# Optimization experiments

Measured on AMD Instinct MI355X. Metric: run time of the kernel, lower is better.

Reference implementation:

```python
import jax, jax.numpy as jnp
import numpy as np

SEQ = 110          # input_size1 = sample_width*2
HALF = SEQ // 2    # 55
N_EMBD = 102       # n_chrom + 2
HEAD = 192

def _cross_half_mask():
    # attention allowed only between the two halves (same-half blocks masked)
    idx = jnp.arange(SEQ)
    same_half = (idx[:, None] < HALF) == (idx[None, :] < HALF)
    return same_half  # True where attention is DISALLOWED

def setup_inputs() -> dict:
    key = jax.random.key(0)
    k1, k2, k3, k4 = jax.random.split(key, 4)
    B = 8192
    x = jax.random.normal(k1, (B, SEQ, N_EMBD), dtype=jnp.float32)
    Wq = jax.random.normal(k2, (N_EMBD, HEAD), dtype=jnp.float32) * (N_EMBD ** -0.5)
    Wk = jax.random.normal(k3, (N_EMBD, HEAD), dtype=jnp.float32) * (N_EMBD ** -0.5)
    Wv = jax.random.normal(k4, (N_EMBD, HEAD), dtype=jnp.float32) * (N_EMBD ** -0.5)
    return {"x": x, "Wq": Wq, "Wk": Wk, "Wv": Wv}

def reference(x, Wq, Wk, Wv):
    # q,k,v: [B, S, H]
    q = x @ Wq
    k = x @ Wk
    v = x @ Wv
    scale = HEAD ** -0.5
    scores = jnp.einsum('bsh,bth->bst', q, k) * scale  # [B, S, S]
    mask = _cross_half_mask()                           # [S, S] True = masked
    scores = jnp.where(mask, -jnp.inf, scores)
    attn = jax.nn.softmax(scores, axis=-1)
    # dropout is identity at inference (p=0.15 at train)
    out = jnp.einsum('bst,bth->bsh', attn, v)           # [B, S, H]
    return out
```

## Files before the change

kernel.cpp:

```cpp
#include <hip/hip_runtime.h>
#include <hip/hip_bf16.h>

#define SEQ   110
#define HALFS 55
#define EMB   102
#define HEAD  192

typedef short bf16x8 __attribute__((ext_vector_type(8)));
typedef float f32x4  __attribute__((ext_vector_type(4)));

#define XS    104
#define XTILE (64 * XS)
#define PS    72
#define MTS   128
#define MTROWS 112
#define MT_SHORTS (MTROWS * MTS)
#define WES   128

__device__ __forceinline__ short f2bf(float f) {
    unsigned u = __float_as_uint(f);
    unsigned r = u + 0x7fffu + ((u >> 16) & 1u);
    return (short)(r >> 16);
}
__device__ __forceinline__ unsigned pk2(float a, float b) {
    return ((unsigned)(unsigned short)f2bf(b) << 16) | (unsigned short)f2bf(a);
}

__global__ void prep(const float* __restrict__ Wq, const float* __restrict__ Wk,
                     const float* __restrict__ Wv, short* __restrict__ ws) {
    int flat = blockIdx.x * 256 + threadIdx.x;
    if (flat < MT_SHORTS) {
        int i = flat >> 7, j = flat & 127;
        float v = 0.0f;
        if (i < EMB && j < EMB) {
            const float4* q4 = (const float4*)(Wq + j * HEAD);
            const float4* k4 = (const float4*)(Wk + i * HEAD);
            float s = 0.0f;
            #pragma unroll 4
            for (int h4 = 0; h4 < HEAD / 4; ++h4) {
                float4 a = q4[h4], b = k4[h4];
                s += a.x * b.x + a.y * b.y + a.z * b.z + a.w * b.w;
            }
            v = s * 0.07216878364870322f;
        }
        ws[flat] = f2bf(v);
    } else if (flat < MT_SHORTS + HEAD * WES) {
        int idx = flat - MT_SHORTS;
        int h = idx >> 7, e = idx & 127;
        float v = (e < EMB) ? Wv[e * HEAD + h] : 0.0f;
        ws[flat] = f2bf(v);
    }
}

__global__ __launch_bounds__(256, 2)
void attn_head(const float* __restrict__ x, const short* __restrict__ ws,
               float* __restrict__ out, int B) {
    const int tid  = threadIdx.x;
    const int w    = tid >> 6;
    const int lane = tid & 63;
    const int g    = lane >> 4;
    const int r    = lane & 15;

    __shared__ __attribute__((aligned(16))) short u[3 * XTILE];
    __shared__ __attribute__((aligned(16))) short P_lds[64 * PS];
    short* slotA = u;
    short* slotB = u + XTILE;
    short* slotC = u + 2 * XTILE;

    const short* Mt  = ws;
    const short* WvT = ws + MT_SHORTS;

    bf16x8 wvf[3][4];
    #pragma unroll
    for (int mi = 0; mi < 3; ++mi) {
        const int hrow = 16 * (w + 4 * mi) + r;
        #pragma unroll
        for (int kk = 0; kk < 4; ++kk)
            wvf[mi][kk] = *(const bf16x8*)(WvT + hrow * WES + 32 * kk + 8 * g);
    }

    {
        unsigned long long* z = (unsigned long long*)u;
        #pragma unroll
        for (int i0 = 0; i0 < 2; ++i0) {
            int ii = tid + i0 * 256;
            if (ii < 468) z[(ii < 234 ? 1430 : 2860) + ii] = 0ull;
        }
        if (tid < 110)
            *(unsigned*)(u + (tid & 1) * XTILE + (tid >> 1) * XS + 102) = 0u;
    }

    unsigned xv0[11], xv1[11];
    auto loadx = [&](int batch) {
        const float4* xb4 = (const float4*)(x + (size_t)batch * (SEQ * EMB));
        #pragma unroll
        for (int it = 0; it < 11; ++it) {
            int i4 = tid + it * 256;
            if (i4 < 2805) { float4 v = xb4[i4]; xv0[it] = pk2(v.x, v.y); xv1[it] = pk2(v.z, v.w); }
        }
    };
    auto stagex = [&]() {
        #pragma unroll
        for (int it = 0; it < 11; ++it) {
            int i4 = tid + it * 256;
            if (i4 < 2805) {
                int fc  = i4 * 4;
                int row = (int)(((unsigned long long)fc * 41121ull) >> 22);
                int e   = fc - row * EMB;
                int tile = row >= HALFS;
                int lr   = row - HALFS * tile;
                int ba   = tile * XTILE + lr * XS + e;
                if (e == 100) {
                    int rowb  = row + 1;
                    int tileb = rowb >= HALFS;
                    int lrb   = rowb - HALFS * tileb;
                    *(unsigned*)(u + ba) = xv0[it];
                    *(unsigned*)(u + tileb * XTILE + lrb * XS) = xv1[it];
                } else {
                    uint2 t2; t2.x = xv0[it]; t2.y = xv1[it];
                    *(uint2*)(u + ba) = t2;
                }
            }
        }
    };

    loadx(blockIdx.x);
    const int stride = (int)gridDim.x;

    bf16x8 ax[4][4];
    bf16x8 zz = {};

    #pragma unroll 1
    for (int p = blockIdx.x; p < B; p += stride) {
        stagex();
        __syncthreads();

        bf16x8 am[2][4];
        #pragma unroll
        for (int mi2 = 0; mi2 < 2; ++mi2) {
            const int mt = w + 4 * mi2;
            #pragma unroll
            for (int kk = 0; kk < 4; ++kk)
                am[mi2][kk] = (mt < 7) ? *(const bf16x8*)(Mt + (16 * mt + r) * MTS + 32 * kk + 8 * g) : zz;
        }

        #pragma unroll
        for (int stl = 0; stl < 4; ++stl) {
            const short* xb = slotA + (16 * stl + r) * XS;
            bf16x8 bx[4];
            #pragma unroll
            for (int kk = 0; kk < 3; ++kk) bx[kk] = *(const bf16x8*)(xb + 32 * kk + 8 * g);
            bx[3] = zz;
            if (g == 0) bx[3] = *(const bf16x8*)(xb + 96);
            #pragma unroll
            for (int mi2 = 0; mi2 < 2; ++mi2) {
                const int mt = w + 4 * mi2;
                if (mt < 7) {
                    f32x4 acc = {0.f, 0.f, 0.f, 0.f};
                    #pragma unroll
                    for (int kk = 0; kk < 4; ++kk)
                        acc = __builtin_amdgcn_mfma_f32_16x16x32_bf16(am[mi2][kk], bx[kk], acc, 0, 0, 0);
                    if (mt < 6 || g < 2) {
                        uint2 t2; t2.x = pk2(acc[0], acc[1]); t2.y = pk2(acc[2], acc[3]);
                        *(uint2*)(slotC + (16 * stl + r) * XS + 16 * mt + 4 * g) = t2;
                    }
                }
            }
        }
        __syncthreads();

        #pragma unroll
        for (int mt = 0; mt < 4; ++mt) {
            const short* xb = slotB + (16 * mt + r) * XS;
            #pragma unroll
            for (int kk = 0; kk < 3; ++kk) ax[mt][kk] = *(const bf16x8*)(xb + 32 * kk + 8 * g);
            ax[mt][3] = zz;
            if (g == 0) ax[mt][3] = *(const bf16x8*)(xb + 96);
        }
        __syncthreads();

        #pragma unroll
        for (int stl = 0; stl < 4; ++stl) {
            #pragma unroll
            for (int mi2 = 0; mi2 < 2; ++mi2) {
                const int mt = w + 4 * mi2;
                if (mt < 7) {
                    f32x4 acc = {0.f, 0.f, 0.f, 0.f};
                    #pragma unroll
                    for (int kk = 0; kk < 4; ++kk)
                        acc = __builtin_amdgcn_mfma_f32_16x16x32_bf16(am[mi2][kk], ax[stl][kk], acc, 0, 0, 0);
                    if (mt < 6 || g < 2) {
                        uint2 t2; t2.x = pk2(acc[0], acc[1]); t2.y = pk2(acc[2], acc[3]);
                        *(uint2*)(slotB + (16 * stl + r) * XS + 16 * mt + 4 * g) = t2;
                    }
                }
            }
        }

        if (p + stride < B) loadx(p + stride);

        const int src0 = ((g & 1) << 5) + r;
        const int src1 = src0 + 16;
        const bool hi  = (g >> 1) != 0;

        #pragma unroll 1
        for (int half = 0; half < 2; ++half) {
            if (half == 1) {
                __syncthreads();
                #pragma unroll
                for (int mt = 0; mt < 4; ++mt) {
                    const short* xb = slotA + (16 * mt + r) * XS;
                    #pragma unroll
                    for (int kk = 0; kk < 3; ++kk) ax[mt][kk] = *(const bf16x8*)(xb + 32 * kk + 8 * g);
                    ax[mt][3] = zz;
                    if (g == 0) ax[mt][3] = *(const bf16x8*)(xb + 96);
                }
            }
            const short* yo = half ? slotB : slotC;

            unsigned vpk[4][3][2];
            #pragma unroll
            for (int st = 0; st < 4; ++st) {
                #pragma unroll
                for (int mi = 0; mi < 3; ++mi) {
                    f32x4 acc = {0.f, 0.f, 0.f, 0.f};
                    #pragma unroll
                    for (int kk = 0; kk < 4; ++kk)
                        acc = __builtin_amdgcn_mfma_f32_16x16x32_bf16(ax[st][kk], wvf[mi][kk], acc, 0, 0, 0);
                    vpk[st][mi][0] = pk2(acc[0], acc[1]);
                    vpk[st][mi][1] = pk2(acc[2], acc[3]);
                }
            }

            bf16x8 va[3][2];
            #pragma unroll
            for (int mi = 0; mi < 3; ++mi) {
                unsigned e00 = (unsigned)__shfl((int)vpk[0][mi][0], src0), e01 = (unsigned)__shfl((int)vpk[0][mi][1], src0);
                unsigned e02 = (unsigned)__shfl((int)vpk[0][mi][0], src1), e03 = (unsigned)__shfl((int)vpk[0][mi][1], src1);
                unsigned f00 = (unsigned)__shfl((int)vpk[1][mi][0], src0), f01 = (unsigned)__shfl((int)vpk[1][mi][1], src0);
                unsigned f02 = (unsigned)__shfl((int)vpk[1][mi][0], src1), f03 = (unsigned)__shfl((int)vpk[1][mi][1], src1);
                uint4 u0;
                u0.x = hi ? f00 : e00; u0.y = hi ? f01 : e01; u0.z = hi ? f02 : e02; u0.w = hi ? f03 : e03;
                unsigned e10 = (unsigned)__shfl((int)vpk[2][mi][0], src0), e11 = (unsigned)__shfl((int)vpk[2][mi][1], src0);
                unsigned e12 = (unsigned)__shfl((int)vpk[2][mi][0], src1), e13 = (unsigned)__shfl((int)vpk[2][mi][1], src1);
                unsigned f10 = (unsigned)__shfl((int)vpk[3][mi][0], src0), f11 = (unsigned)__shfl((int)vpk[3][mi][1], src0);
                unsigned f12 = (unsigned)__shfl((int)vpk[3][mi][0], src1), f13 = (unsigned)__shfl((int)vpk[3][mi][1], src1);
                uint4 u1;
                u1.x = hi ? f10 : e10; u1.y = hi ? f11 : e11; u1.z = hi ? f12 : e12; u1.w = hi ? f13 : e13;
                __builtin_memcpy(&va[mi][0], &u0, 16);
                __builtin_memcpy(&va[mi][1], &u1, 16);
            }

            {
                const short* yb = yo + (16 * w + r) * XS;
                bf16x8 by[4];
                #pragma unroll
                for (int kk = 0; kk < 3; ++kk) by[kk] = *(const bf16x8*)(yb + 32 * kk + 8 * g);
                by[3] = zz;
                if (g == 0) by[3] = *(const bf16x8*)(yb + 96);

                float sc[4][4];
                #pragma unroll
                for (int mt = 0; mt < 4; ++mt) {
                    f32x4 acc = {0.f, 0.f, 0.f, 0.f};
                    #pragma unroll
                    for (int kk = 0; kk < 4; ++kk)
                        acc = __builtin_amdgcn_mfma_f32_16x16x32_bf16(ax[mt][kk], by[kk], acc, 0, 0, 0);
                    #pragma unroll
                    for (int j = 0; j < 4; ++j) sc[mt][j] = acc[j];
                }
                #pragma unroll
                for (int j = 0; j < 4; ++j)
                    if (48 + 4 * g + j >= HALFS) sc[3][j] = -1e30f;

                float mx = -1e30f;
                #pragma unroll
                for (int mt = 0; mt < 4; ++mt) {
                    #pragma unroll
                    for (int j = 0; j < 4; ++j) mx = fmaxf(mx, sc[mt][j]);
                }
                mx = fmaxf(mx, __shfl_xor(mx, 16));
                mx = fmaxf(mx, __shfl_xor(mx, 32));
                float pr[4][4];
                float sum = 0.f;
                #pragma unroll
                for (int mt = 0; mt < 4; ++mt) {
                    #pragma unroll
                    for (int j = 0; j < 4; ++j) { pr[mt][j] = __expf(sc[mt][j] - mx); sum += pr[mt][j]; }
                }
                sum += __shfl_xor(sum, 16);
                sum += __shfl_xor(sum, 32);
                float rs = 1.0f / sum;

                #pragma unroll
                for (int mt = 0; mt < 4; ++mt) {
                    uint2 t2;
                    t2.x = pk2(pr[mt][0] * rs, pr[mt][1] * rs);
                    t2.y = pk2(pr[mt][2] * rs, pr[mt][3] * rs);
                    *(uint2*)(P_lds + (16 * w + r) * PS + 16 * mt + 4 * g) = t2;
                }
            }
            __syncthreads();

            const size_t obase = (size_t)p * (SEQ * HEAD) + (size_t)(half * HALFS) * HEAD;
            #pragma unroll
            for (int c = 0; c < 4; ++c) {
                const short* pb = P_lds + (16 * c + r) * PS + 8 * g;
                bf16x8 bp0 = *(const bf16x8*)(pb);
                bf16x8 bp1 = *(const bf16x8*)(pb + 32);
                const int srow  = 16 * c + r;
                const bool valid = srow < HALFS;
                float* orow = out + obase + (size_t)srow * HEAD;
                #pragma unroll
                for (int mi = 0; mi < 3; ++mi) {
                    f32x4 acc = {0.f, 0.f, 0.f, 0.f};
                    acc = __builtin_amdgcn_mfma_f32_16x16x32_bf16(va[mi][0], bp0, acc, 0, 0, 0);
                    acc = __builtin_amdgcn_mfma_f32_16x16x32_bf16(va[mi][1], bp1, acc, 0, 0, 0);
                    if (valid) {
                        float4 st4; st4.x = acc[0]; st4.y = acc[1]; st4.z = acc[2]; st4.w = acc[3];
                        *(float4*)(orow + 16 * (w + 4 * mi) + 4 * g) = st4;
                    }
                }
            }
        }
        __syncthreads();
    }
}

extern "C" void kernel_launch(void* const* d_in, const int* in_sizes, int n_in,
                              void* d_out, int out_size, void* d_ws, size_t ws_size,
                              hipStream_t stream) {
    const float* x  = (const float*)d_in[0];
    const float* Wq = (const float*)d_in[1];
    const float* Wk = (const float*)d_in[2];
    const float* Wv = (const float*)d_in[3];
    short* ws = (short*)d_ws;
    int B = in_sizes[0] / (SEQ * EMB);
    int prep_elems = MT_SHORTS + HEAD * WES;
    prep<<<(prep_elems + 255) / 256, 256, 0, stream>>>(Wq, Wk, Wv, ws);
    attn_head<<<512, 256, 0, stream>>>(x, ws, (float*)d_out, B);
}
```

Baseline: 336.3 us.

## Process both sequence halves concurrently with 512-thread blocks, one 4-wave group per half

Doubles the block to 8 waves and gives each group of 4 waves one half of the sequence. The two halves' projection, score, softmax and output stages now run in parallel instead of in a serial two-pass loop, which removes several barriers and the serialized half loop. LDS grows by one extra x tile and a second probability buffer. The launch bound of 512 threads with 4 blocks per unit may force register pressure and spills, because each thread still holds large fragment arrays.

```diff
diff --git a/kernel.cpp b/kernel.cpp
--- a/kernel.cpp
+++ b/kernel.cpp
@@ -52,20 +52,24 @@
     }
 }
 
-__global__ __launch_bounds__(256, 2)
+__global__ __launch_bounds__(512, 4)
 void attn_head(const float* __restrict__ x, const short* __restrict__ ws,
                float* __restrict__ out, int B) {
     const int tid  = threadIdx.x;
-    const int w    = tid >> 6;
+    const int w8   = tid >> 6;
+    const int h    = w8 >> 2;
+    const int w4   = w8 & 3;
     const int lane = tid & 63;
     const int g    = lane >> 4;
     const int r    = lane & 15;
 
-    __shared__ __attribute__((aligned(16))) short u[3 * XTILE];
-    __shared__ __attribute__((aligned(16))) short P_lds[64 * PS];
-    short* slotA = u;
-    short* slotB = u + XTILE;
-    short* slotC = u + 2 * XTILE;
+    __shared__ __attribute__((aligned(16))) short u[4 * XTILE];
+    __shared__ __attribute__((aligned(16))) short P_lds[2][64 * PS];
+
+    short* xh = u + h * XTILE;
+    short* xo = u + (h ^ 1) * XTILE;
+    short* yh = u + (2 + h) * XTILE;
+    short* Ph = P_lds[h];
 
     const short* Mt  = ws;
     const short* WvT = ws + MT_SHORTS;
@@ -73,7 +77,7 @@
     bf16x8 wvf[3][4];
     #pragma unroll
     for (int mi = 0; mi < 3; ++mi) {
-        const int hrow = 16 * (w + 4 * mi) + r;
+        const int hrow = 16 * (w4 + 4 * mi) + r;
         #pragma unroll
         for (int kk = 0; kk < 4; ++kk)
             wvf[mi][kk] = *(const bf16x8*)(WvT + hrow * WES + 32 * kk + 8 * g);
@@ -81,28 +85,24 @@
 
     {
         unsigned long long* z = (unsigned long long*)u;
-        #pragma unroll
-        for (int i0 = 0; i0 < 2; ++i0) {
-            int ii = tid + i0 * 256;
-            if (ii < 468) z[(ii < 234 ? 1430 : 2860) + ii] = 0ull;
-        }
+        if (tid < 468) z[(tid < 234 ? 1430 : 2860) + tid] = 0ull;
         if (tid < 110)
             *(unsigned*)(u + (tid & 1) * XTILE + (tid >> 1) * XS + 102) = 0u;
     }
 
-    unsigned xv0[11], xv1[11];
+    unsigned xv0[6], xv1[6];
     auto loadx = [&](int batch) {
         const float4* xb4 = (const float4*)(x + (size_t)batch * (SEQ * EMB));
         #pragma unroll
-        for (int it = 0; it < 11; ++it) {
-            int i4 = tid + it * 256;
+        for (int it = 0; it < 6; ++it) {
+            int i4 = tid + it * 512;
             if (i4 < 2805) { float4 v = xb4[i4]; xv0[it] = pk2(v.x, v.y); xv1[it] = pk2(v.z, v.w); }
         }
     };
     auto stagex = [&]() {
         #pragma unroll
-        for (int it = 0; it < 11; ++it) {
-            int i4 = tid + it * 256;
+        for (int it = 0; it < 6; ++it) {
+            int i4 = tid + it * 512;
             if (i4 < 2805) {
                 int fc  = i4 * 4;
                 int row = (int)(((unsigned long long)fc * 41121ull) >> 22);
@@ -138,7 +138,7 @@
         bf16x8 am[2][4];
         #pragma unroll
         for (int mi2 = 0; mi2 < 2; ++mi2) {
-            const int mt = w + 4 * mi2;
+            const int mt = w4 + 4 * mi2;
             #pragma unroll
             for (int kk = 0; kk < 4; ++kk)
                 am[mi2][kk] = (mt < 7) ? *(const bf16x8*)(Mt + (16 * mt + r) * MTS + 32 * kk + 8 * g) : zz;
@@ -146,7 +146,7 @@
 
         #pragma unroll
         for (int stl = 0; stl < 4; ++stl) {
-            const short* xb = slotA + (16 * stl + r) * XS;
+            const short* xb = xh + (16 * stl + r) * XS;
             bf16x8 bx[4];
             #pragma unroll
             for (int kk = 0; kk < 3; ++kk) bx[kk] = *(const bf16x8*)(xb + 32 * kk + 8 * g);
@@ -154,7 +154,7 @@
             if (g == 0) bx[3] = *(const bf16x8*)(xb + 96);
             #pragma unroll
             for (int mi2 = 0; mi2 < 2; ++mi2) {
-                const int mt = w + 4 * mi2;
+                const int mt = w4 + 4 * mi2;
                 if (mt < 7) {
                     f32x4 acc = {0.f, 0.f, 0.f, 0.f};
                     #pragma unroll
@@ -162,164 +162,128 @@
                         acc = __builtin_amdgcn_mfma_f32_16x16x32_bf16(am[mi2][kk], bx[kk], acc, 0, 0, 0);
                     if (mt < 6 || g < 2) {
                         uint2 t2; t2.x = pk2(acc[0], acc[1]); t2.y = pk2(acc[2], acc[3]);
-                        *(uint2*)(slotC + (16 * stl + r) * XS + 16 * mt + 4 * g) = t2;
+                        *(uint2*)(yh + (16 * stl + r) * XS + 16 * mt + 4 * g) = t2;
                     }
                 }
             }
         }
-        __syncthreads();
 
         #pragma unroll
         for (int mt = 0; mt < 4; ++mt) {
-            const short* xb = slotB + (16 * mt + r) * XS;
+            const short* xb = xo + (16 * mt + r) * XS;
             #pragma unroll
             for (int kk = 0; kk < 3; ++kk) ax[mt][kk] = *(const bf16x8*)(xb + 32 * kk + 8 * g);
             ax[mt][3] = zz;
             if (g == 0) ax[mt][3] = *(const bf16x8*)(xb + 96);
         }
-        __syncthreads();
-
-        #pragma unroll
-        for (int stl = 0; stl < 4; ++stl) {
-            #pragma unroll
-            for (int mi2 = 0; mi2 < 2; ++mi2) {
-                const int mt = w + 4 * mi2;
-                if (mt < 7) {
-                    f32x4 acc = {0.f, 0.f, 0.f, 0.f};
-                    #pragma unroll
-                    for (int kk = 0; kk < 4; ++kk)
-                        acc = __builtin_amdgcn_mfma_f32_16x16x32_bf16(am[mi2][kk], ax[stl][kk], acc, 0, 0, 0);
-                    if (mt < 6 || g < 2) {
-                        uint2 t2; t2.x = pk2(acc[0], acc[1]); t2.y = pk2(acc[2], acc[3]);
-                        *(uint2*)(slotB + (16 * stl + r) * XS + 16 * mt + 4 * g) = t2;
-                    }
-                }
-            }
-        }
-
-        if (p + stride < B) loadx(p + stride);
-
+
+        unsigned vpk[4][3][2];
+        #pragma unroll
+        for (int st = 0; st < 4; ++st) {
+            #pragma unroll
+            for (int mi = 0; mi < 3; ++mi) {
+                f32x4 acc = {0.f, 0.f, 0.f, 0.f};
+                #pragma unroll
+                for (int kk = 0; kk < 4; ++kk)
+                    acc = __builtin_amdgcn_mfma_f32_16x16x32_bf16(ax[st][kk], wvf[mi][kk], acc, 0, 0, 0);
+                vpk[st][mi][0] = pk2(acc[0], acc[1]);
+                vpk[st][mi][1] = pk2(acc[2], acc[3]);
+            }
+        }
         const int src0 = ((g & 1) << 5) + r;
         const int src1 = src0 + 16;
         const bool hi  = (g >> 1) != 0;
-
-        #pragma unroll 1
-        for (int half = 0; half < 2; ++half) {
-            if (half == 1) {
-                __syncthreads();
-                #pragma unroll
-                for (int mt = 0; mt < 4; ++mt) {
-                    const short* xb = slotA + (16 * mt + r) * XS;
-                    #pragma unroll
-                    for (int kk = 0; kk < 3; ++kk) ax[mt][kk] = *(const bf16x8*)(xb + 32 * kk + 8 * g);
-                    ax[mt][3] = zz;
-                    if (g == 0) ax[mt][3] = *(const bf16x8*)(xb + 96);
-                }
-            }
-            const short* yo = half ? slotB : slotC;
-
-            unsigned vpk[4][3][2];
-            #pragma unroll
-            for (int st = 0; st < 4; ++st) {
-                #pragma unroll
-                for (int mi = 0; mi < 3; ++mi) {
-                    f32x4 acc = {0.f, 0.f, 0.f, 0.f};
-                    #pragma unroll
-                    for (int kk = 0; kk < 4; ++kk)
-                        acc = __builtin_amdgcn_mfma_f32_16x16x32_bf16(ax[st][kk], wvf[mi][kk], acc, 0, 0, 0);
-                    vpk[st][mi][0] = pk2(acc[0], acc[1]);
-                    vpk[st][mi][1] = pk2(acc[2], acc[3]);
-                }
-            }
-
-            bf16x8 va[3][2];
+        bf16x8 va[3][2];
+        #pragma unroll
+        for (int mi = 0; mi < 3; ++mi) {
+            unsigned e00 = (unsigned)__shfl((int)vpk[0][mi][0], src0), e01 = (unsigned)__shfl((int)vpk[0][mi][1], src0);
+            unsigned e02 = (unsigned)__shfl((int)vpk[0][mi][0], src1), e03 = (unsigned)__shfl((int)vpk[0][mi][1], src1);
+            unsigned f00 = (unsigned)__shfl((int)vpk[1][mi][0], src0), f01 = (unsigned)__shfl((int)vpk[1][mi][1], src0);
+            unsigned f02 = (unsigned)__shfl((int)vpk[1][mi][0], src1), f03 = (unsigned)__shfl((int)vpk[1][mi][1], src1);
+            uint4 u0;
+            u0.x = hi ? f00 : e00; u0.y = hi ? f01 : e01; u0.z = hi ? f02 : e02; u0.w = hi ? f03 : e03;
+            unsigned e10 = (unsigned)__shfl((int)vpk[2][mi][0], src0), e11 = (unsigned)__shfl((int)vpk[2][mi][1], src0);
+            unsigned e12 = (unsigned)__shfl((int)vpk[2][mi][0], src1), e13 = (unsigned)__shfl((int)vpk[2][mi][1], src1);
+            unsigned f10 = (unsigned)__shfl((int)vpk[3][mi][0], src0), f11 = (unsigned)__shfl((int)vpk[3][mi][1], src0);
+            unsigned f12 = (unsigned)__shfl((int)vpk[3][mi][0], src1), f13 = (unsigned)__shfl((int)vpk[3][mi][1], src1);
+            uint4 u1;
+            u1.x = hi ? f10 : e10; u1.y = hi ? f11 : e11; u1.z = hi ? f12 : e12; u1.w = hi ? f13 : e13;
+            __builtin_memcpy(&va[mi][0], &u0, 16);
+            __builtin_memcpy(&va[mi][1], &u1, 16);
+        }
+
+        __syncthreads();
+
+        if (p + stride < B) loadx(p + stride);
+
+        {
+            const short* yb = yh + (16 * w4 + r) * XS;
+            bf16x8 by[4];
+            #pragma unroll
+            for (int kk = 0; kk < 3; ++kk) by[kk] = *(const bf16x8*)(yb + 32 * kk + 8 * g);
+            by[3] = zz;
+            if (g == 0) by[3] = *(const bf16x8*)(yb + 96);
+
+            float sc[4][4];
+            #pragma unroll
+            for (int mt = 0; mt < 4; ++mt) {
+                f32x4 acc = {0.f, 0.f, 0.f, 0.f};
+                #pragma unroll
+                for (int kk = 0; kk < 4; ++kk)
+                    acc = __builtin_amdgcn_mfma_f32_16x16x32_bf16(ax[mt][kk], by[kk], acc, 0, 0, 0);
+                #pragma unroll
+                for (int j = 0; j < 4; ++j) sc[mt][j] = acc[j];
+            }
+            #pragma unroll
+            for (int j = 0; j < 4; ++j)
+                if (48 + 4 * g + j >= HALFS) sc[3][j] = -1e30f;
+
+            float mx = -1e30f;
+            #pragma unroll
+            for (int mt = 0; mt < 4; ++mt) {
+                #pragma unroll
+                for (int j = 0; j < 4; ++j) mx = fmaxf(mx, sc[mt][j]);
+            }
+            mx = fmaxf(mx, __shfl_xor(mx, 16));
+            mx = fmaxf(mx, __shfl_xor(mx, 32));
+            float pr[4][4];
+            float sum = 0.f;
+            #pragma unroll
+            for (int mt = 0; mt < 4; ++mt) {
+                #pragma unroll
+                for (int j = 0; j < 4; ++j) { pr[mt][j] = __expf(sc[mt][j] - mx); sum += pr[mt][j]; }
+            }
+            sum += __shfl_xor(sum, 16);
+            sum += __shfl_xor(sum, 32);
+            float rs = 1.0f / sum;
+
+            #pragma unroll
+            for (int mt = 0; mt < 4; ++mt) {
+                uint2 t2;
+                t2.x = pk2(pr[mt][0] * rs, pr[mt][1] * rs);
+                t2.y = pk2(pr[mt][2] * rs, pr[mt][3] * rs);
+                *(uint2*)(Ph + (16 * w4 + r) * PS + 16 * mt + 4 * g) = t2;
+            }
+        }
+        __syncthreads();
+
+        const size_t obase = (size_t)p * (SEQ * HEAD) + (size_t)(h * HALFS) * HEAD;
+        #pragma unroll
+        for (int c = 0; c < 4; ++c) {
+            const short* pb = Ph + (16 * c + r) * PS + 8 * g;
+            bf16x8 bp0 = *(const bf16x8*)(pb);
+            bf16x8 bp1 = *(const bf16x8*)(pb + 32);
+            const int srow  = 16 * c + r;
+            const bool valid = srow < HALFS;
+            float* orow = out + obase + (size_t)srow * HEAD;
             #pragma unroll
             for (int mi = 0; mi < 3; ++mi) {
-                unsigned e00 = (unsigned)__shfl((int)vpk[0][mi][0], src0), e01 = (unsigned)__shfl((int)vpk[0][mi][1], src0);
-                unsigned e02 = (unsigned)__shfl((int)vpk[0][mi][0], src1), e03 = (unsigned)__shfl((int)vpk[0][mi][1], src1);
-                unsigned f00 = (unsigned)__shfl((int)vpk[1][mi][0], src0), f01 = (unsigned)__shfl((int)vpk[1][mi][1], src0);
-                unsigned f02 = (unsigned)__shfl((int)vpk[1][mi][0], src1), f03 = (unsigned)__shfl((int)vpk[1][mi][1], src1);
-                uint4 u0;
-                u0.x = hi ? f00 : e00; u0.y = hi ? f01 : e01; u0.z = hi ? f02 : e02; u0.w = hi ? f03 : e03;
-                unsigned e10 = (unsigned)__shfl((int)vpk[2][mi][0], src0), e11 = (unsigned)__shfl((int)vpk[2][mi][1], src0);
-                unsigned e12 = (unsigned)__shfl((int)vpk[2][mi][0], src1), e13 = (unsigned)__shfl((int)vpk[2][mi][1], src1);
-                unsigned f10 = (unsigned)__shfl((int)vpk[3][mi][0], src0), f11 = (unsigned)__shfl((int)vpk[3][mi][1], src0);
-                unsigned f12 = (unsigned)__shfl((int)vpk[3][mi][0], src1), f13 = (unsigned)__shfl((int)vpk[3][mi][1], src1);
-                uint4 u1;
-                u1.x = hi ? f10 : e10; u1.y = hi ? f11 : e11; u1.z = hi ? f12 : e12; u1.w = hi ? f13 : e13;
-                __builtin_memcpy(&va[mi][0], &u0, 16);
-                __builtin_memcpy(&va[mi][1], &u1, 16);
-            }
-
-            {
-                const short* yb = yo + (16 * w + r) * XS;
-                bf16x8 by[4];
-                #pragma unroll
-                for (int kk = 0; kk < 3; ++kk) by[kk] = *(const bf16x8*)(yb + 32 * kk + 8 * g);
-                by[3] = zz;
-                if (g == 0) by[3] = *(const bf16x8*)(yb + 96);
-
-                float sc[4][4];
-                #pragma unroll
-                for (int mt = 0; mt < 4; ++mt) {
-                    f32x4 acc = {0.f, 0.f, 0.f, 0.f};
-                    #pragma unroll
-                    for (int kk = 0; kk < 4; ++kk)
-                        acc = __builtin_amdgcn_mfma_f32_16x16x32_bf16(ax[mt][kk], by[kk], acc, 0, 0, 0);
-                    #pragma unroll
-                    for (int j = 0; j < 4; ++j) sc[mt][j] = acc[j];
-                }
-                #pragma unroll
-                for (int j = 0; j < 4; ++j)
-                    if (48 + 4 * g + j >= HALFS) sc[3][j] = -1e30f;
-
-                float mx = -1e30f;
-                #pragma unroll
-                for (int mt = 0; mt < 4; ++mt) {
-                    #pragma unroll
-                    for (int j = 0; j < 4; ++j) mx = fmaxf(mx, sc[mt][j]);
-                }
-                mx = fmaxf(mx, __shfl_xor(mx, 16));
-                mx = fmaxf(mx, __shfl_xor(mx, 32));
-                float pr[4][4];
-                float sum = 0.f;
-                #pragma unroll
-                for (int mt = 0; mt < 4; ++mt) {
-                    #pragma unroll
-                    for (int j = 0; j < 4; ++j) { pr[mt][j] = __expf(sc[mt][j] - mx); sum += pr[mt][j]; }
-                }
-                sum += __shfl_xor(sum, 16);
-                sum += __shfl_xor(sum, 32);
-                float rs = 1.0f / sum;
-
-                #pragma unroll
-                for (int mt = 0; mt < 4; ++mt) {
-                    uint2 t2;
-                    t2.x = pk2(pr[mt][0] * rs, pr[mt][1] * rs);
-                    t2.y = pk2(pr[mt][2] * rs, pr[mt][3] * rs);
-                    *(uint2*)(P_lds + (16 * w + r) * PS + 16 * mt + 4 * g) = t2;
-                }
-            }
-            __syncthreads();
-
-            const size_t obase = (size_t)p * (SEQ * HEAD) + (size_t)(half * HALFS) * HEAD;
-            #pragma unroll
-            for (int c = 0; c < 4; ++c) {
-                const short* pb = P_lds + (16 * c + r) * PS + 8 * g;
-                bf16x8 bp0 = *(const bf16x8*)(pb);
-                bf16x8 bp1 = *(const bf16x8*)(pb + 32);
-                const int srow  = 16 * c + r;
-                const bool valid = srow < HALFS;
-                float* orow = out + obase + (size_t)srow * HEAD;
-                #pragma unroll
-                for (int mi = 0; mi < 3; ++mi) {
-                    f32x4 acc = {0.f, 0.f, 0.f, 0.f};
-                    acc = __builtin_amdgcn_mfma_f32_16x16x32_bf16(va[mi][0], bp0, acc, 0, 0, 0);
-                    acc = __builtin_amdgcn_mfma_f32_16x16x32_bf16(va[mi][1], bp1, acc, 0, 0, 0);
-                    if (valid) {
-                        float4 st4; st4.x = acc[0]; st4.y = acc[1]; st4.z = acc[2]; st4.w = acc[3];
-                        *(float4*)(orow + 16 * (w + 4 * mi) + 4 * g) = st4;
-                    }
+                f32x4 acc = {0.f, 0.f, 0.f, 0.f};
+                acc = __builtin_amdgcn_mfma_f32_16x16x32_bf16(va[mi][0], bp0, acc, 0, 0, 0);
+                acc = __builtin_amdgcn_mfma_f32_16x16x32_bf16(va[mi][1], bp1, acc, 0, 0, 0);
+                if (valid) {
+                    float4 st4; st4.x = acc[0]; st4.y = acc[1]; st4.z = acc[2]; st4.w = acc[3];
+                    *(float4*)(orow + 16 * (w4 + 4 * mi) + 4 * g) = st4;
                 }
             }
         }
@@ -338,5 +302,5 @@
     int B = in_sizes[0] / (SEQ * EMB);
     int prep_elems = MT_SHORTS + HEAD * WES;
     prep<<<(prep_elems + 255) / 256, 256, 0, stream>>>(Wq, Wk, Wv, ws);
-    attn_head<<<512, 256, 0, stream>>>(x, ws, (float*)d_out, B);
-}
+    attn_head<<<512, 512, 0, stream>>>(x, ws, (float*)d_out, B);
+}
```

Measured after the change: 963.6 us. 186% more time.
